# Optimization experiments

Hardware: AMD Instinct MI355X
Metric: run time of the kernel (lower is better)

Reference implementation:

```python
import jax, jax.numpy as jnp
import numpy as np

STEP_NUM = 2
NEG_INF = -1e10


def _walked_edges(edges, step_num):
    # Faithful recursion from GraphLayer._get_walked_edges.
    # step_num <= 1 returns edges unthresholded; deeper levels threshold > 0.
    if step_num <= 1:
        return edges
    deeper = _walked_edges(jnp.einsum('bij,bjk->bik', edges, edges), step_num // 2)
    if step_num % 2 == 1:
        deeper = deeper + edges
    return (deeper > 0.0).astype(edges.dtype)


def setup_inputs() -> dict:
    key = jax.random.key(0)
    k1, k2 = jax.random.split(key)
    B, N, D = 4, 1024, 32
    features = jax.random.normal(k1, (B, N, D), dtype=jnp.float32)
    edges = jax.random.randint(k2, (B, N, N), 0, 2, dtype=jnp.int32)
    return {"features": features, "edges": edges}


def reference(features, edges):
    # features: [B, N, D], edges: [B, N, N] dense adjacency (0/1)
    e = edges.astype(features.dtype)
    if STEP_NUM > 1:
        e = _walked_edges(e, STEP_NUM)
    # GraphMaxPool semantics: out[b,i,:] = max_j (feat[b,j,:] + (1-e[b,i,j])*NEG_INF)
    masked = features[:, None, :, :] + (1.0 - e)[:, :, :, None] * NEG_INF  # [B,N,N,D]
    return jnp.max(masked, axis=2)
```

## Files before the change

kernel.cpp:

```cpp
#include <hip/hip_runtime.h>
#include <cstdint>

#define BB 4
#define NN 1024
#define DD 32
#define NWORDS 16
#define RPB 16
#define NEG_INF_F (-1e10f)

typedef unsigned long long u64;

#define TILE_OFF  0
#define WORD0_OFF (BB * 64 * NWORDS)
#define CPART_OFF ((BB * 64 * NWORDS + BB * NN) * 2)

__global__ __launch_bounds__(256, 1) void prep_kernel(
        const float* __restrict__ feat,
        const int*   __restrict__ edges,
        u64*         __restrict__ ws64,
        float*       __restrict__ wsf) {
    const int blk = blockIdx.x;
    const int t   = threadIdx.x;

    __shared__ u64 s_word[NWORDS];
    __shared__ __align__(16) float4 s_red[32 * 8];

    if (blk < 256) {
        const int4 v = reinterpret_cast<const int4*>(
            edges + (size_t)blk * NN
        )[0];
        const size_t grow = (size_t)(blk >> 6) * NN + (blk & 63);
        const int4 vv = reinterpret_cast<const int4*>(edges + grow * NN)[t];
        (void)v;
        const unsigned nib = (vv.x != 0 ? 1u : 0u) | (vv.y != 0 ? 2u : 0u)
                           | (vv.z != 0 ? 4u : 0u) | (vv.w != 0 ? 8u : 0u);
        if (t < NWORDS) s_word[t] = 0ull;
        __syncthreads();
        atomicOr(&s_word[t >> 4], (u64)nib << ((t & 15) * 4));
        __syncthreads();
        if (t < NWORDS) ws64[TILE_OFF + blk * NWORDS + t] = s_word[t];
    } else if (blk < 512) {
        const int idx  = blk - 256;
        const int grow = idx * 16 + (t >> 4);
        const int4 vv = reinterpret_cast<const int4*>(
            edges + (size_t)grow * NN)[t & 15];
        const unsigned nib = (vv.x != 0 ? 1u : 0u) | (vv.y != 0 ? 2u : 0u)
                           | (vv.z != 0 ? 4u : 0u) | (vv.w != 0 ? 8u : 0u);
        if (t < NWORDS) s_word[t] = 0ull;
        __syncthreads();
        atomicOr(&s_word[t >> 4], (u64)nib << ((t & 15) * 4));
        __syncthreads();
        if (t < NWORDS) ws64[WORD0_OFF + idx * 16 + t] = s_word[t];
    } else {
        const int p    = blk - 512;
        const int b    = p >> 4;
        const int part = p & 15;
        const float4* fb4 = reinterpret_cast<const float4*>(
            feat + (size_t)b * NN * DD);
        const int d4 = t & 7;
        const int kc = t >> 3;
        float4 m = make_float4(-INFINITY, -INFINITY, -INFINITY, -INFINITY);
#pragma unroll
        for (int kk = 0; kk < 2; ++kk) {
            const float4 v2 = fb4[(size_t)(part * 64 + kc * 2 + kk) * 8 + d4];
            m.x = fmaxf(m.x, v2.x); m.y = fmaxf(m.y, v2.y);
            m.z = fmaxf(m.z, v2.z); m.w = fmaxf(m.w, v2.w);
        }
        s_red[kc * 8 + d4] = m;
        __syncthreads();
        for (int s = 16; s > 0; s >>= 1) {
            if (t < s * 8) {
                float4 a = s_red[t];
                const float4 c = s_red[t + s * 8];
                a.x = fmaxf(a.x, c.x); a.y = fmaxf(a.y, c.y);
                a.z = fmaxf(a.z, c.z); a.w = fmaxf(a.w, c.w);
                s_red[t] = a;
            }
            __syncthreads();
        }
        if (t < 8)
            reinterpret_cast<float4*>(wsf + CPART_OFF + (b * 16 + part) * DD)[t]
                = s_red[t];
    }
}

__global__ __launch_bounds__(256, 1) void pool_kernel(
        const float* __restrict__ feat,
        const int*   __restrict__ edges,
        const u64*   __restrict__ ws64,
        const float* __restrict__ wsf,
        float*       __restrict__ out) {
    const int blk = blockIdx.x;
    const int b   = blk >> 6;
    const int r0  = (blk & 63) * RPB;
    const int t   = threadIdx.x;
    const int il  = t >> 4;
    const int w   = t & 15;

    __shared__ __align__(16) u64 s_tile[64 * NWORDS];
    __shared__ u64   s_rw[RPB];
    __shared__ int   s_need[RPB];
    __shared__ float s_part[256];
    __shared__ int           s_ei[NN];
    __shared__ unsigned char s_reach[NN];
    __shared__ float s_m[256], s_u[256];

    if (t < RPB) s_need[t] = 0;

    {
        const longlong2* tb = reinterpret_cast<const longlong2*>(
            ws64 + TILE_OFF + (size_t)b * 64 * NWORDS);
        reinterpret_cast<longlong2*>(s_tile)[t]       = tb[t];
        reinterpret_cast<longlong2*>(s_tile)[t + 256] = tb[t + 256];
    }
    if (t < RPB) s_rw[t] = ws64[WORD0_OFF + b * NN + r0 + t];
    {
        const float* cp = wsf + CPART_OFF + (size_t)b * 16 * DD;
        s_part[t] = fmaxf(cp[t], cp[t + 256]);
    }
    __syncthreads();
    for (int s = 128; s >= 32; s >>= 1) {
        if (t < s) s_part[t] = fmaxf(s_part[t], s_part[t + s]);
        __syncthreads();
    }

    {
        const u64 nb = s_rw[il];
        u64 acc = 0ull;
#pragma unroll
        for (int j = 0; j < 64; ++j) {
            const u64 msk = 0ull - ((nb >> j) & 1ull);
            acc |= s_tile[j * NWORDS + w] & msk;
        }
        if (acc != ~0ull) atomicAdd(&s_need[il], 1);
    }
    __syncthreads();

    float* orow_base = out + (size_t)(b * NN + r0) * DD;
    if (s_need[il] == 0) {
        reinterpret_cast<float2*>(orow_base + il * DD)[w] =
            reinterpret_cast<const float2*>(s_part)[w];
    }

    bool any = false;
    for (int r = 0; r < RPB; ++r) any = any || (s_need[r] != 0);
    if (!any) return;

    const int* eb = edges + (size_t)b * NN * NN;
    for (int r = 0; r < RPB; ++r) {
        if (s_need[r] == 0) continue;
        const int i = r0 + r;
        const int* ei = eb + (size_t)i * NN;
#pragma unroll
        for (int q = 0; q < 4; ++q) s_ei[t + q * 256] = ei[t + q * 256];
        __syncthreads();
#pragma unroll
        for (int kq = 0; kq < 4; ++kq) {
            const int k = t * 4 + kq;
            int reach = 0;
            for (int j = 0; j < NN; ++j) {
                if (s_ei[j] != 0 && eb[(size_t)j * NN + k] != 0) { reach = 1; break; }
            }
            s_reach[k] = (unsigned char)reach;
        }
        __syncthreads();
        const int d   = t & 31;
        const int kc8 = t >> 5;
        const float* fb = feat + (size_t)b * NN * DD;
        float mm = -INFINITY, um = -INFINITY;
        for (int kk = 0; kk < 128; ++kk) {
            const int k = kc8 * 128 + kk;
            const float f = fb[(size_t)k * DD + d];
            if (s_reach[k]) mm = fmaxf(mm, f); else um = fmaxf(um, f);
        }
        s_m[t] = mm; s_u[t] = um;
        __syncthreads();
        for (int s = 4; s > 0; s >>= 1) {
            if (kc8 < s) {
                s_m[kc8 * 32 + d] = fmaxf(s_m[kc8 * 32 + d], s_m[(kc8 + s) * 32 + d]);
                s_u[kc8 * 32 + d] = fmaxf(s_u[kc8 * 32 + d], s_u[(kc8 + s) * 32 + d]);
            }
            __syncthreads();
        }
        if (kc8 == 0)
            out[(size_t)(b * NN + i) * DD + d] = fmaxf(s_m[d], s_u[d] + NEG_INF_F);
        __syncthreads();
    }
}

extern "C" void kernel_launch(void* const* d_in, const int* in_sizes, int n_in,
                              void* d_out, int out_size, void* d_ws, size_t ws_size,
                              hipStream_t stream) {
    const float* feat  = (const float*)d_in[0];
    const int*   edges = (const int*)d_in[1];
    float*       out   = (float*)d_out;
    u64*   ws64 = (u64*)d_ws;
    float* wsf  = (float*)d_ws;

    prep_kernel<<<576, 256, 0, stream>>>(feat, edges, ws64, wsf);
    pool_kernel<<<BB * NN / RPB, 256, 0, stream>>>(feat, edges, ws64, wsf, out);
}
```

Baseline: 69.25 us.

## Fuse edge-bitmask prep and feature max into a single pooling kernel

Drops the separate prep kernel and its workspace round trip. Each pooling block now builds its own 64-row adjacency bitmask with wavefront ballots and computes the per-batch feature max itself. This removes one kernel launch and the global-memory handoff between the two kernels. In exchange, every block redundantly reads 256 KB of edges and the whole batch's features, which adds L2 traffic.

```diff
diff --git a/kernel.cpp b/kernel.cpp
--- a/kernel.cpp
+++ b/kernel.cpp
@@ -10,122 +10,78 @@
 
 typedef unsigned long long u64;
 
-#define TILE_OFF  0
-#define WORD0_OFF (BB * 64 * NWORDS)
-#define CPART_OFF ((BB * 64 * NWORDS + BB * NN) * 2)
-
-__global__ __launch_bounds__(256, 1) void prep_kernel(
+__global__ __launch_bounds__(256, 1) void fused_kernel(
         const float* __restrict__ feat,
         const int*   __restrict__ edges,
-        u64*         __restrict__ ws64,
-        float*       __restrict__ wsf) {
-    const int blk = blockIdx.x;
-    const int t   = threadIdx.x;
+        float*       __restrict__ out) {
+    const int blk  = blockIdx.x;
+    const int b    = blk >> 6;
+    const int r0   = (blk & 63) * RPB;
+    const int t    = threadIdx.x;
+    const int lane = t & 63;
+    const int wid  = t >> 6;
 
-    __shared__ u64 s_word[NWORDS];
-    __shared__ __align__(16) float4 s_red[32 * 8];
-
-    if (blk < 256) {
-        const int4 v = reinterpret_cast<const int4*>(
-            edges + (size_t)blk * NN
-        )[0];
-        const size_t grow = (size_t)(blk >> 6) * NN + (blk & 63);
-        const int4 vv = reinterpret_cast<const int4*>(edges + grow * NN)[t];
-        (void)v;
-        const unsigned nib = (vv.x != 0 ? 1u : 0u) | (vv.y != 0 ? 2u : 0u)
-                           | (vv.z != 0 ? 4u : 0u) | (vv.w != 0 ? 8u : 0u);
-        if (t < NWORDS) s_word[t] = 0ull;
-        __syncthreads();
-        atomicOr(&s_word[t >> 4], (u64)nib << ((t & 15) * 4));
-        __syncthreads();
-        if (t < NWORDS) ws64[TILE_OFF + blk * NWORDS + t] = s_word[t];
-    } else if (blk < 512) {
-        const int idx  = blk - 256;
-        const int grow = idx * 16 + (t >> 4);
-        const int4 vv = reinterpret_cast<const int4*>(
-            edges + (size_t)grow * NN)[t & 15];
-        const unsigned nib = (vv.x != 0 ? 1u : 0u) | (vv.y != 0 ? 2u : 0u)
-                           | (vv.z != 0 ? 4u : 0u) | (vv.w != 0 ? 8u : 0u);
-        if (t < NWORDS) s_word[t] = 0ull;
-        __syncthreads();
-        atomicOr(&s_word[t >> 4], (u64)nib << ((t & 15) * 4));
-        __syncthreads();
-        if (t < NWORDS) ws64[WORD0_OFF + idx * 16 + t] = s_word[t];
-    } else {
-        const int p    = blk - 512;
-        const int b    = p >> 4;
-        const int part = p & 15;
-        const float4* fb4 = reinterpret_cast<const float4*>(
-            feat + (size_t)b * NN * DD);
-        const int d4 = t & 7;
-        const int kc = t >> 3;
-        float4 m = make_float4(-INFINITY, -INFINITY, -INFINITY, -INFINITY);
-#pragma unroll
-        for (int kk = 0; kk < 2; ++kk) {
-            const float4 v2 = fb4[(size_t)(part * 64 + kc * 2 + kk) * 8 + d4];
-            m.x = fmaxf(m.x, v2.x); m.y = fmaxf(m.y, v2.y);
-            m.z = fmaxf(m.z, v2.z); m.w = fmaxf(m.w, v2.w);
-        }
-        s_red[kc * 8 + d4] = m;
-        __syncthreads();
-        for (int s = 16; s > 0; s >>= 1) {
-            if (t < s * 8) {
-                float4 a = s_red[t];
-                const float4 c = s_red[t + s * 8];
-                a.x = fmaxf(a.x, c.x); a.y = fmaxf(a.y, c.y);
-                a.z = fmaxf(a.z, c.z); a.w = fmaxf(a.w, c.w);
-                s_red[t] = a;
-            }
-            __syncthreads();
-        }
-        if (t < 8)
-            reinterpret_cast<float4*>(wsf + CPART_OFF + (b * 16 + part) * DD)[t]
-                = s_red[t];
-    }
-}
-
-__global__ __launch_bounds__(256, 1) void pool_kernel(
-        const float* __restrict__ feat,
-        const int*   __restrict__ edges,
-        const u64*   __restrict__ ws64,
-        const float* __restrict__ wsf,
-        float*       __restrict__ out) {
-    const int blk = blockIdx.x;
-    const int b   = blk >> 6;
-    const int r0  = (blk & 63) * RPB;
-    const int t   = threadIdx.x;
-    const int il  = t >> 4;
-    const int w   = t & 15;
-
-    __shared__ __align__(16) u64 s_tile[64 * NWORDS];
-    __shared__ u64   s_rw[RPB];
+    __shared__ u64   s_tile[64 * NWORDS];
+    __shared__ u64   s_nb[RPB];
     __shared__ int   s_need[RPB];
-    __shared__ float s_part[256];
+    __shared__ __align__(16) float4 s_red[256];
     __shared__ int           s_ei[NN];
     __shared__ unsigned char s_reach[NN];
     __shared__ float s_m[256], s_u[256];
 
     if (t < RPB) s_need[t] = 0;
 
+    const int* eb = edges + (size_t)b * NN * NN;
+
     {
-        const longlong2* tb = reinterpret_cast<const longlong2*>(
-            ws64 + TILE_OFF + (size_t)b * 64 * NWORDS);
-        reinterpret_cast<longlong2*>(s_tile)[t]       = tb[t];
-        reinterpret_cast<longlong2*>(s_tile)[t + 256] = tb[t + 256];
+        const int* rp = eb + (size_t)(wid * 16) * NN + lane;
+#pragma unroll 2
+        for (int jj = 0; jj < 16; ++jj) {
+            const int j = wid * 16 + jj;
+#pragma unroll
+            for (int w = 0; w < NWORDS; ++w) {
+                const int v = rp[(size_t)jj * NN + w * 64];
+                const u64 bal = __ballot(v != 0);
+                if (lane == 0) s_tile[j * NWORDS + w] = bal;
+            }
+        }
     }
-    if (t < RPB) s_rw[t] = ws64[WORD0_OFF + b * NN + r0 + t];
+
+#pragma unroll
+    for (int q = 0; q < 4; ++q) {
+        const int rr = wid * 4 + q;
+        const int v  = eb[(size_t)(r0 + rr) * NN + lane];
+        const u64 bal = __ballot(v != 0);
+        if (lane == 0) s_nb[rr] = bal;
+    }
+
     {
-        const float* cp = wsf + CPART_OFF + (size_t)b * 16 * DD;
-        s_part[t] = fmaxf(cp[t], cp[t + 256]);
+        const float4* fb4 = reinterpret_cast<const float4*>(feat + (size_t)b * NN * DD);
+        float4 m = make_float4(-INFINITY, -INFINITY, -INFINITY, -INFINITY);
+#pragma unroll 8
+        for (int kk = 0; kk < 32; ++kk) {
+            const float4 v = fb4[(size_t)kk * 256 + t];
+            m.x = fmaxf(m.x, v.x); m.y = fmaxf(m.y, v.y);
+            m.z = fmaxf(m.z, v.z); m.w = fmaxf(m.w, v.w);
+        }
+        s_red[t] = m;
     }
     __syncthreads();
-    for (int s = 128; s >= 32; s >>= 1) {
-        if (t < s) s_part[t] = fmaxf(s_part[t], s_part[t + s]);
+    for (int s = 16; s > 0; s >>= 1) {
+        if (t < s * 8) {
+            float4 a = s_red[t];
+            const float4 c = s_red[t + s * 8];
+            a.x = fmaxf(a.x, c.x); a.y = fmaxf(a.y, c.y);
+            a.z = fmaxf(a.z, c.z); a.w = fmaxf(a.w, c.w);
+            s_red[t] = a;
+        }
         __syncthreads();
     }
 
+    const int il = t >> 4;
+    const int w  = t & 15;
     {
-        const u64 nb = s_rw[il];
+        const u64 nb = s_nb[il];
         u64 acc = 0ull;
 #pragma unroll
         for (int j = 0; j < 64; ++j) {
@@ -139,14 +95,14 @@
     float* orow_base = out + (size_t)(b * NN + r0) * DD;
     if (s_need[il] == 0) {
         reinterpret_cast<float2*>(orow_base + il * DD)[w] =
-            reinterpret_cast<const float2*>(s_part)[w];
+            reinterpret_cast<const float2*>(s_red)[w];
     }
 
     bool any = false;
+#pragma unroll
     for (int r = 0; r < RPB; ++r) any = any || (s_need[r] != 0);
     if (!any) return;
 
-    const int* eb = edges + (size_t)b * NN * NN;
     for (int r = 0; r < RPB; ++r) {
         if (s_need[r] == 0) continue;
         const int i = r0 + r;
@@ -194,9 +150,7 @@
     const float* feat  = (const float*)d_in[0];
     const int*   edges = (const int*)d_in[1];
     float*       out   = (float*)d_out;
-    u64*   ws64 = (u64*)d_ws;
-    float* wsf  = (float*)d_ws;
+    (void)d_ws; (void)ws_size;
 
-    prep_kernel<<<576, 256, 0, stream>>>(feat, edges, ws64, wsf);
-    pool_kernel<<<BB * NN / RPB, 256, 0, stream>>>(feat, edges, ws64, wsf, out);
+    fused_kernel<<<BB * 64, 256, 0, stream>>>(feat, edges, out);
 }
```

After: 131.8 us. 1.9x slower.
